# Kernel optimization log

Measured on AMD Instinct MI355X. Metric: run time of the kernel, lower is better.

## Reference

```python
import jax, jax.numpy as jnp
import numpy as np

DIM = 512
NUM_HEADS = 8
HEAD_DIM = DIM // NUM_HEADS
SCALE = HEAD_DIM ** -0.5


def setup_inputs() -> dict:
    key = jax.random.key(0)
    ks = jax.random.split(key, 11)
    B, T, D = 2, 4096, DIM
    s = 0.02
    return {
        "query": jax.random.normal(ks[0], (B, T, D), jnp.float32),
        "key_": jax.random.normal(ks[1], (B, T, D), jnp.float32),
        "value": jax.random.normal(ks[2], (B, T, D), jnp.float32),
        "Wq": jax.random.normal(ks[3], (D, D), jnp.float32) * s,
        "bq": jnp.zeros((D,), jnp.float32),
        "Wk": jax.random.normal(ks[4], (D, D), jnp.float32) * s,
        "bk": jnp.zeros((D,), jnp.float32),
        "Wv": jax.random.normal(ks[5], (D, D), jnp.float32) * s,
        "bv": jnp.zeros((D,), jnp.float32),
        "Wo": jax.random.normal(ks[6], (D, D), jnp.float32) * s,
        "bo": jnp.zeros((D,), jnp.float32),
    }


def reference(query, key_, value, Wq, bq, Wk, bk, Wv, bv, Wo, bo):
    B, T, D = query.shape
    H, Hd = NUM_HEADS, HEAD_DIM
    # Linear projections (torch Linear: x @ W.T + b)
    q = (query @ Wq.T + bq).reshape(B, T, H, Hd).transpose(0, 2, 1, 3)   # [B,H,T,Hd]
    k = (key_ @ Wk.T + bk).reshape(B, -1, H, Hd).transpose(0, 2, 1, 3)    # [B,H,S,Hd]
    v = (value @ Wv.T + bv).reshape(B, -1, H, Hd).transpose(0, 2, 1, 3)   # [B,H,S,Hd]
    # Full O(T*S) score matrix, as in the original (non-fused) module
    scores = jnp.einsum("bhtd,bhsd->bhts", q, k) * SCALE                  # [B,H,T,S]
    weights = jax.nn.softmax(scores, axis=-1)
    out = jnp.einsum("bhts,bhsd->bhtd", weights, v)                       # [B,H,T,Hd]
    out = out.transpose(0, 2, 1, 3).reshape(B, T, D)
    return out @ Wo.T + bo
```

## Files before the change

kernel.cpp:

```cpp
#include <hip/hip_runtime.h>
#include <cstdint>
#include <cstddef>

typedef __attribute__((ext_vector_type(8)))  __bf16 bf16x8;
typedef __attribute__((ext_vector_type(4)))  float  f32x4;
typedef __attribute__((ext_vector_type(16))) float  f32x16;
typedef __attribute__((ext_vector_type(8)))  unsigned short us8;

#define MFMA(a, b, c)   __builtin_amdgcn_mfma_f32_16x16x32_bf16((a), (b), (c), 0, 0, 0)
#define MFMA32(a, b, c) __builtin_amdgcn_mfma_f32_32x32x16_bf16((a), (b), (c), 0, 0, 0)

#define QSCALE 0.18033688011112042f

__device__ __forceinline__ unsigned short f2bf(float f) {
  unsigned u = __float_as_uint(f);
  u += 0x7fffu + ((u >> 16) & 1u);
  return (unsigned short)(u >> 16);
}

__device__ __forceinline__ float bf2f(unsigned short s) {
  unsigned u = ((unsigned)s) << 16;
  return __uint_as_float(u);
}

__device__ __forceinline__ unsigned cvtpk(float lo, float hi) {
  unsigned r;
  asm("v_cvt_pk_bf16_f32 %0, %1, %2" : "=v"(r) : "v"(lo), "v"(hi));
  return r;
}

__device__ __forceinline__ void pl32swap(unsigned& a, unsigned& b) {
  asm("v_permlane32_swap_b32 %0, %1" : "+v"(a), "+v"(b));
}

__device__ __forceinline__ void gload16(const void* g, void* l) {
  __builtin_amdgcn_global_load_lds(
      (__attribute__((address_space(1))) unsigned int*)(uintptr_t)g,
      (__attribute__((address_space(3))) unsigned int*)l,
      16, 0, 0);
}

__device__ __forceinline__ float tree16(const float* p) {
  float a = (p[0] + p[1]) + (p[2] + p[3]);
  float b = (p[4] + p[5]) + (p[6] + p[7]);
  float c = (p[8] + p[9]) + (p[10] + p[11]);
  float d = (p[12] + p[13]) + (p[14] + p[15]);
  return (a + b) + (c + d);
}

struct CastArgs {
  const float*    src[7];
  unsigned short* dst[7];
};
__global__ __launch_bounds__(256) void cast_kernel(CastArgs a) {
  const int i = blockIdx.x * 256 + threadIdx.x;
  int z, off;
  if (i < 3145728) { z = i >> 20;            off = i & 1048575; }
  else             { int j = i - 3145728; z = 3 + (j >> 16); off = j & 65535; }
  float4 f = ((const float4*)a.src[z])[off];
  ushort4 r;
  r.x = f2bf(f.x); r.y = f2bf(f.y); r.z = f2bf(f.z); r.w = f2bf(f.w);
  ((ushort4*)a.dst[z])[off] = r;
}

struct ProjArgs {
  const unsigned short* X[3];
  const unsigned short* W[3];
  const float*          bias[3];
  unsigned short*       out[3];
};

__global__ __launch_bounds__(256) void proj_qkv_kernel(ProjArgs args) {
  __shared__ alignas(16) unsigned short smem[3 * 8192];

  const int z = blockIdx.z;
  const unsigned short* __restrict__ X   = args.X[z];
  const unsigned short* __restrict__ W   = args.W[z];
  const float* __restrict__ bias         = args.bias[z];
  unsigned short* __restrict__ out       = args.out[z];
  const float scl = (z == 0) ? QSCALE : 1.0f;

  const int t = threadIdx.x;
  const int w = t >> 6, lane = t & 63;
  const int quad = lane >> 4, l15 = lane & 15;
  const int wr = w >> 1, wc = w & 1;
  const int m0 = blockIdx.x * 128, n0 = blockIdx.y * 128;

  const int srow = t >> 2;
  const int scol = (((t & 3) ^ (srow & 3)) << 3);

  f32x4 acc[4][4] = {};

#define STAGEP(idx, kk)                                                        \
  {                                                                            \
    unsigned short* nA = smem + (idx) * 8192;                                  \
    unsigned short* nB = nA + 4096;                                            \
    gload16(X + (size_t)(m0 + srow) * 512 + (kk) + scol,      &nA[w * 512]);   \
    gload16(X + (size_t)(m0 + srow + 64) * 512 + (kk) + scol, &nA[2048 + w * 512]); \
    gload16(W + (size_t)(n0 + srow) * 512 + (kk) + scol,      &nB[w * 512]);   \
    gload16(W + (size_t)(n0 + srow + 64) * 512 + (kk) + scol, &nB[2048 + w * 512]); \
  }

  STAGEP(0, 0);
  STAGEP(1, 32);

#pragma unroll
  for (int k0 = 0; k0 < 512; k0 += 32) {
    const int bi = (k0 >> 5) % 3;
    unsigned short* sA = smem + bi * 8192;
    unsigned short* sB = sA + 4096;
    if (k0 < 448) {
      STAGEP((bi + 2) % 3, k0 + 64);
      asm volatile("s_waitcnt vmcnt(8)" ::: "memory");
    } else if (k0 == 448) {
      asm volatile("s_waitcnt vmcnt(4)" ::: "memory");
    } else {
      asm volatile("s_waitcnt vmcnt(0)" ::: "memory");
    }
    __builtin_amdgcn_s_barrier();
    asm volatile("" ::: "memory");

    bf16x8 af[4], bfr[4];
#pragma unroll
    for (int mt = 0; mt < 4; ++mt) {
      int ra = wr * 64 + mt * 16 + l15;
      af[mt] = *(const bf16x8*)&sA[ra * 32 + ((quad ^ (ra & 3)) << 3)];
    }
#pragma unroll
    for (int nt = 0; nt < 4; ++nt) {
      int rb = wc * 64 + nt * 16 + l15;
      bfr[nt] = *(const bf16x8*)&sB[rb * 32 + ((quad ^ (rb & 3)) << 3)];
    }
#pragma unroll
    for (int mt = 0; mt < 4; ++mt)
#pragma unroll
      for (int nt = 0; nt < 4; ++nt)
        acc[mt][nt] = MFMA(af[mt], bfr[nt], acc[mt][nt]);

    asm volatile("" ::: "memory");
    __builtin_amdgcn_s_barrier();
  }
#undef STAGEP

  if (z != 2) {
#pragma unroll
    for (int nt = 0; nt < 4; ++nt) {
      int n = n0 + wc * 64 + nt * 16 + l15;
      float bv = bias[n];
      int h = n >> 6, hd = n & 63;
#pragma unroll
      for (int mt = 0; mt < 4; ++mt) {
#pragma unroll
        for (int r = 0; r < 4; ++r) {
          int m = m0 + wr * 64 + mt * 16 + quad * 4 + r;
          int b = m >> 12, tt = m & 4095;
          out[(((size_t)(b * 8 + h)) * 4096 + tt) * 64 + hd] =
              f2bf((acc[mt][nt][r] + bv) * scl);
        }
      }
    }
  } else {
    const int b   = m0 >> 12;
    const int tt0 = m0 & 4095;
#pragma unroll
    for (int h2 = 0; h2 < 2; ++h2) {
      __syncthreads();
      if (wc == h2) {
#pragma unroll
        for (int nt = 0; nt < 4; ++nt) {
          int nl = nt * 16 + l15;
          float bv = bias[n0 + h2 * 64 + nl];
#pragma unroll
          for (int mt = 0; mt < 4; ++mt)
#pragma unroll
            for (int r = 0; r < 4; ++r) {
              int ml = wr * 64 + mt * 16 + quad * 4 + r;
              smem[nl * 136 + ml] = f2bf((acc[mt][nt][r] + bv) * scl);
            }
        }
      }
      __syncthreads();
      const int row = t >> 2;
      const int c4  = (t & 3) * 8;
      const int n   = n0 + h2 * 64 + row;
      unsigned short* dst = out + ((size_t)(b * 512 + n)) * 4096 + tt0;
#pragma unroll
      for (int k = 0; k < 4; ++k)
        *(us8*)(dst + c4 + k * 32) = *(const us8*)&smem[row * 136 + c4 + k * 32];
    }
  }
}

__global__ __launch_bounds__(256) void proj_out_kernel(
    const unsigned short* __restrict__ P0, const unsigned short* __restrict__ P1,
    const float* __restrict__ pL, const unsigned short* __restrict__ W,
    const float* __restrict__ bias, float* __restrict__ out) {
  __shared__ alignas(16) unsigned short sA[2][2048];
  __shared__ alignas(16) unsigned short sB[3][4096];
  __shared__ float invL[512];

  const int t = threadIdx.x;
  const int w = t >> 6, lane = t & 63;
  const int quad = lane >> 4, l15 = lane & 15;
  const int m0 = blockIdx.x * 64, n0 = blockIdx.y * 128;
  const int b  = m0 >> 12, tt0 = m0 & 4095;

  {
    const int hh = t >> 5;
    const int r2 = (t & 31) * 2;
#pragma unroll
    for (int i = 0; i < 2; ++i) {
      const int row = r2 + i;
      const size_t ix = (size_t)(b * 8 + hh) * 4096 + tt0 + row;
      invL[hh * 64 + row] = 1.0f / (pL[ix] + pL[65536 + ix]);
    }
  }

  const int arow = t >> 2, ac = t & 3;
  const int srow = t >> 2;
  const int scol = (((t & 3) ^ (srow & 3)) << 3);

  __syncthreads();

  {
    us8 a0 = *(const us8*)&P0[(size_t)(m0 + arow) * 512 + ac * 8];
    us8 a1 = *(const us8*)&P1[(size_t)(m0 + arow) * 512 + ac * 8];
    const float inv = invL[arow];
    unsigned o[4];
#pragma unroll
    for (int i = 0; i < 4; ++i)
      o[i] = cvtpk((bf2f(a0[2 * i]) + bf2f(a1[2 * i])) * inv,
                   (bf2f(a0[2 * i + 1]) + bf2f(a1[2 * i + 1])) * inv);
    *(us8*)&sA[0][arow * 32 + ((ac ^ (arow & 3)) << 3)] = *(us8*)o;
    gload16(W + (size_t)(n0 + srow) * 512 + scol,      &sB[0][w * 512]);
    gload16(W + (size_t)(n0 + srow + 64) * 512 + scol, &sB[0][2048 + w * 512]);
    gload16(W + (size_t)(n0 + srow) * 512 + 32 + scol,      &sB[1][w * 512]);
    gload16(W + (size_t)(n0 + srow + 64) * 512 + 32 + scol, &sB[1][2048 + w * 512]);
  }
  __syncthreads();

  f32x4 acc[4][2] = {};

#pragma unroll
  for (int k0 = 0; k0 < 512; k0 += 32) {
    const int ba = (k0 >> 5) & 1;
    const int bb = (k0 >> 5) % 3;

    us8 a0n = {}, a1n = {};
    float invn = 0.f;
    if (k0 < 480) {
      const int kn = k0 + 32;
      a0n = *(const us8*)&P0[(size_t)(m0 + arow) * 512 + kn + ac * 8];
      a1n = *(const us8*)&P1[(size_t)(m0 + arow) * 512 + kn + ac * 8];
      invn = invL[(kn >> 6) * 64 + arow];
    }
    if (k0 < 448) {
      const int kn2 = k0 + 64;
      gload16(W + (size_t)(n0 + srow) * 512 + kn2 + scol,      &sB[(bb + 2) % 3][w * 512]);
      gload16(W + (size_t)(n0 + srow + 64) * 512 + kn2 + scol, &sB[(bb + 2) % 3][2048 + w * 512]);
    }

    bf16x8 af[4], bfr[2];
#pragma unroll
    for (int mt = 0; mt < 4; ++mt) {
      int ra = mt * 16 + l15;
      af[mt] = *(const bf16x8*)&sA[ba][ra * 32 + ((quad ^ (ra & 3)) << 3)];
    }
#pragma unroll
    for (int nt = 0; nt < 2; ++nt) {
      int rb = w * 32 + nt * 16 + l15;
      bfr[nt] = *(const bf16x8*)&sB[bb][rb * 32 + ((quad ^ (rb & 3)) << 3)];
    }
#pragma unroll
    for (int mt = 0; mt < 4; ++mt)
#pragma unroll
      for (int nt = 0; nt < 2; ++nt)
        acc[mt][nt] = MFMA(af[mt], bfr[nt], acc[mt][nt]);

    if (k0 < 480) {
      unsigned o[4];
#pragma unroll
      for (int i = 0; i < 4; ++i)
        o[i] = cvtpk((bf2f(a0n[2 * i]) + bf2f(a1n[2 * i])) * invn,
                     (bf2f(a0n[2 * i + 1]) + bf2f(a1n[2 * i + 1])) * invn);
      *(us8*)&sA[ba ^ 1][arow * 32 + ((ac ^ (arow & 3)) << 3)] = *(us8*)o;
    }

    asm volatile("s_waitcnt vmcnt(2) lgkmcnt(0)" ::: "memory");
    __builtin_amdgcn_s_barrier();
  }

#pragma unroll
  for (int nt = 0; nt < 2; ++nt) {
    int n = n0 + w * 32 + nt * 16 + l15;
    float bv = bias[n];
#pragma unroll
    for (int mt = 0; mt < 4; ++mt) {
#pragma unroll
      for (int r = 0; r < 4; ++r) {
        int m = m0 + mt * 16 + quad * 4 + r;
        out[(size_t)m * 512 + n] = acc[mt][nt][r] + bv;
      }
    }
  }
}

__global__ __launch_bounds__(128, 2) void attn_kernel(
    const unsigned short* __restrict__ Q, const unsigned short* __restrict__ K,
    const unsigned short* __restrict__ VT,
    unsigned short* __restrict__ pO0, unsigned short* __restrict__ pO1,
    float* __restrict__ pL) {
  __shared__ alignas(16) unsigned short kt[2][4096];
  __shared__ alignas(16) unsigned short vt[2][4096];

  const int t = threadIdx.x;
  const int w = t >> 6;
  const int lane = t & 63;
  const int l31 = lane & 31, h = lane >> 5;

  const int wg  = blockIdx.x + gridDim.x * blockIdx.y;
  const int swz = (wg & 7) * 128 + (wg >> 3);
  const int qt  = swz & 31;
  const int bh2 = swz >> 5;
  const int bh  = bh2 & 15, half = bh2 >> 4;

  const unsigned short* __restrict__ Qp  = Q  + (size_t)bh * 4096 * 64;
  const unsigned short* __restrict__ Kp  = K  + (size_t)bh * 4096 * 64;
  const unsigned short* __restrict__ VTp = VT + (size_t)bh * 64 * 4096;

  const int q0w = qt * 128 + w * 64;
  const int sbase = half * 2048;

  const int lr   = lane >> 3;
  const int gcol = (((lane & 7) ^ lr) << 3);

#define STAGE(bbuf, s0)                                                        \
  {                                                                            \
    _Pragma("unroll")                                                          \
    for (int i = 0; i < 4; ++i)                                                \
      gload16(Kp + (size_t)((s0) + w * 32 + i * 8 + lr) * 64 + gcol,           \
              &kt[bbuf][(w * 32 + i * 8) * 64]);                               \
    _Pragma("unroll")                                                          \
    for (int i = 0; i < 4; ++i)                                                \
      gload16(VTp + (size_t)(w * 32 + i * 8 + lr) * 4096 + (s0) + gcol,        \
              &vt[bbuf][(w * 32 + i * 8) * 64]);                               \
  }

  STAGE(0, sbase);

  bf16x8 aqA[4], aqB[4];
#pragma unroll
  for (int kd = 0; kd < 4; ++kd) {
    aqA[kd] = *(const bf16x8*)(Qp + (size_t)(q0w + l31) * 64 + kd * 16 + h * 8);
    aqB[kd] = *(const bf16x8*)(Qp + (size_t)(q0w + 32 + l31) * 64 + kd * 16 + h * 8);
  }

  f32x16 o0a = {}, o1a = {}, o0b = {}, o1b = {};
  float lia = 0.f, lib = 0.f;

  const int swzk = l31 & 7;

  for (int j = 0; j < 32; ++j) {
    const int cb = j & 1, nb = cb ^ 1;
    if (j < 31) {
      STAGE(nb, sbase + (j + 1) * 64);
      asm volatile("s_waitcnt vmcnt(8)" ::: "memory");
    } else {
      asm volatile("s_waitcnt vmcnt(0)" ::: "memory");
    }
    __builtin_amdgcn_s_barrier();
    asm volatile("" ::: "memory");

    const unsigned short* ktb = kt[cb];
    const unsigned short* vtb = vt[cb];

#pragma unroll
    for (int st = 0; st < 2; ++st) {
      bf16x8 kf[4];
#pragma unroll
      for (int kd = 0; kd < 4; ++kd)
        kf[kd] = *(const bf16x8*)&ktb[(st * 32 + l31) * 64 +
                                      (((2 * kd + h) ^ swzk) << 3)];
      f32x16 sa = {}, sb = {};
      __builtin_amdgcn_s_setprio(1);
#pragma unroll
      for (int kd = 0; kd < 4; ++kd) {
        sa = MFMA32(kf[kd], aqA[kd], sa);
        sb = MFMA32(kf[kd], aqB[kd], sb);
      }
      __builtin_amdgcn_s_setprio(0);

      float pA[16], pB[16];
#pragma unroll
      for (int r = 0; r < 16; ++r) {
        pA[r] = __builtin_amdgcn_exp2f(sa[r]);
        pB[r] = __builtin_amdgcn_exp2f(sb[r]);
      }
      lia += tree16(pA);
      lib += tree16(pB);

      unsigned XgA[4], YgA[4], XgB[4], YgB[4];
#pragma unroll
      for (int g = 0; g < 4; ++g) {
        XgA[g] = cvtpk(pA[4 * g + 0], pA[4 * g + 1]);
        YgA[g] = cvtpk(pA[4 * g + 2], pA[4 * g + 3]);
        XgB[g] = cvtpk(pB[4 * g + 0], pB[4 * g + 1]);
        YgB[g] = cvtpk(pB[4 * g + 2], pB[4 * g + 3]);
      }

      __builtin_amdgcn_s_setprio(1);
#pragma unroll
      for (int ks = 0; ks < 2; ++ks) {
        const int c = st * 4 + 2 * ks + h;
        bf16x8 v0 = *(const bf16x8*)&vtb[l31 * 64 + ((c ^ swzk) << 3)];
        bf16x8 v1 = *(const bf16x8*)&vtb[(l31 + 32) * 64 + ((c ^ swzk) << 3)];

        unsigned a0 = XgA[2 * ks], a2 = XgA[2 * ks + 1];
        unsigned a1 = YgA[2 * ks], a3 = YgA[2 * ks + 1];
        pl32swap(a0, a2);
        pl32swap(a1, a3);
        union { unsigned u[4]; bf16x8 v; } paA;
        paA.u[0] = a0; paA.u[1] = a1; paA.u[2] = a2; paA.u[3] = a3;
        o0a = MFMA32(paA.v, v0, o0a);
        o1a = MFMA32(paA.v, v1, o1a);

        unsigned b0 = XgB[2 * ks], b2 = XgB[2 * ks + 1];
        unsigned b1 = YgB[2 * ks], b3 = YgB[2 * ks + 1];
        pl32swap(b0, b2);
        pl32swap(b1, b3);
        union { unsigned u[4]; bf16x8 v; } paB;
        paB.u[0] = b0; paB.u[1] = b1; paB.u[2] = b2; paB.u[3] = b3;
        o0b = MFMA32(paB.v, v0, o0b);
        o1b = MFMA32(paB.v, v1, o1b);
      }
      __builtin_amdgcn_s_setprio(0);
    }

    asm volatile("" ::: "memory");
    __builtin_amdgcn_s_barrier();
  }
#undef STAGE

  lia += __shfl_xor(lia, 32, 64);
  lib += __shfl_xor(lib, 32, 64);
  float* __restrict__ PLh = pL + half * 65536 + bh * 4096;
  if (h == 0) {
    PLh[q0w + l31]      = lia;
    PLh[q0w + 32 + l31] = lib;
  }

  unsigned short* __restrict__ PO = half ? pO1 : pO0;
  const int bq = bh >> 3, hh = bh & 7;
#pragma unroll
  for (int r = 0; r < 16; ++r) {
    const int qloc = (r & 3) + 8 * (r >> 2) + 4 * h;
    const size_t baseA = ((size_t)bq * 4096 + q0w + qloc) * 512 + hh * 64;
    PO[baseA + l31]      = f2bf(o0a[r]);
    PO[baseA + 32 + l31] = f2bf(o1a[r]);
    const size_t baseB = ((size_t)bq * 4096 + q0w + 32 + qloc) * 512 + hh * 64;
    PO[baseB + l31]      = f2bf(o0b[r]);
    PO[baseB + 32 + l31] = f2bf(o1b[r]);
  }
}

extern "C" void kernel_launch(void* const* d_in, const int* in_sizes, int n_in,
                              void* d_out, int out_size, void* d_ws, size_t ws_size,
                              hipStream_t stream) {
  (void)in_sizes; (void)n_in; (void)out_size; (void)ws_size;
  const float* query = (const float*)d_in[0];
  const float* key_  = (const float*)d_in[1];
  const float* value = (const float*)d_in[2];
  const float* Wq = (const float*)d_in[3];
  const float* bq = (const float*)d_in[4];
  const float* Wk = (const float*)d_in[5];
  const float* bk = (const float*)d_in[6];
  const float* Wv = (const float*)d_in[7];
  const float* bv = (const float*)d_in[8];
  const float* Wo = (const float*)d_in[9];
  const float* bo = (const float*)d_in[10];
  float* out = (float*)d_out;

  char* ws = (char*)d_ws;
  const size_t MB = 1024 * 1024;
  unsigned short* Xq  = (unsigned short*)(ws + 0 * MB);
  unsigned short* Xk  = (unsigned short*)(ws + 8 * MB);
  unsigned short* Xv  = (unsigned short*)(ws + 16 * MB);
  unsigned short* Wqb = (unsigned short*)(ws + 24 * MB);
  unsigned short* Wkb = (unsigned short*)(ws + 24 * MB + 512 * 1024);
  unsigned short* Wvb = (unsigned short*)(ws + 25 * MB);
  unsigned short* qb  = (unsigned short*)(ws + 26 * MB);
  unsigned short* kb  = (unsigned short*)(ws + 34 * MB);
  unsigned short* vtb = (unsigned short*)(ws + 42 * MB);
  unsigned short* Wob = (unsigned short*)(ws + 58 * MB);
  unsigned short* pO0 = (unsigned short*)(ws + 0 * MB);
  unsigned short* pO1 = (unsigned short*)(ws + 9 * MB);
  float*          pL  = (float*)(ws + 18 * MB);

  CastArgs ca;
  ca.src[0] = query; ca.src[1] = key_; ca.src[2] = value;
  ca.src[3] = Wq;    ca.src[4] = Wk;   ca.src[5] = Wv;  ca.src[6] = Wo;
  ca.dst[0] = Xq;    ca.dst[1] = Xk;   ca.dst[2] = Xv;
  ca.dst[3] = Wqb;   ca.dst[4] = Wkb;  ca.dst[5] = Wvb; ca.dst[6] = Wob;
  cast_kernel<<<dim3(13312), 256, 0, stream>>>(ca);

  ProjArgs pa;
  pa.X[0] = Xq;  pa.X[1] = Xk;  pa.X[2] = Xv;
  pa.W[0] = Wqb; pa.W[1] = Wkb; pa.W[2] = Wvb;
  pa.bias[0] = bq; pa.bias[1] = bk; pa.bias[2] = bv;
  pa.out[0] = qb; pa.out[1] = kb; pa.out[2] = vtb;
  proj_qkv_kernel<<<dim3(64, 4, 3), 256, 0, stream>>>(pa);

  attn_kernel<<<dim3(32, 32), 128, 0, stream>>>(qb, kb, vtb, pO0, pO1, pL);

  proj_out_kernel<<<dim3(128, 4), 256, 0, stream>>>(pO0, pO1, pL, Wob, bo, out);
}
```

Baseline: 219.6 us.

## Fuse fp32-to-bf16 activation cast into QKV projection loads

The separate cast kernel no longer converts the large query/key/value activations. The projection kernel instead loads fp32 rows directly through registers, converts them to bf16 and writes them into a double-buffered LDS tile, while weights keep async global-to-LDS loads in a triple buffer. This removes a full write and re-read of the bf16 activation copies, at the cost of doubled fp32 global reads per tile and register-staged writes that may expose latency. The attention kernel's s_setprio raises around its MFMA blocks are also removed.

```diff
diff --git a/kernel.cpp b/kernel.cpp
--- a/kernel.cpp
+++ b/kernel.cpp
@@ -49,14 +49,12 @@
 }
 
 struct CastArgs {
-  const float*    src[7];
-  unsigned short* dst[7];
+  const float*    src[4];
+  unsigned short* dst[4];
 };
 __global__ __launch_bounds__(256) void cast_kernel(CastArgs a) {
   const int i = blockIdx.x * 256 + threadIdx.x;
-  int z, off;
-  if (i < 3145728) { z = i >> 20;            off = i & 1048575; }
-  else             { int j = i - 3145728; z = 3 + (j >> 16); off = j & 65535; }
+  const int z = i >> 16, off = i & 65535;
   float4 f = ((const float4*)a.src[z])[off];
   ushort4 r;
   r.x = f2bf(f.x); r.y = f2bf(f.y); r.z = f2bf(f.z); r.w = f2bf(f.w);
@@ -64,17 +62,19 @@
 }
 
 struct ProjArgs {
-  const unsigned short* X[3];
+  const float*          Xf[3];
   const unsigned short* W[3];
   const float*          bias[3];
   unsigned short*       out[3];
 };
 
 __global__ __launch_bounds__(256) void proj_qkv_kernel(ProjArgs args) {
-  __shared__ alignas(16) unsigned short smem[3 * 8192];
+  __shared__ alignas(16) unsigned short smem[20480];
+  unsigned short* sAb[2] = {smem, smem + 4096};
+  unsigned short* sBb[3] = {smem + 8192, smem + 12288, smem + 16384};
 
   const int z = blockIdx.z;
-  const unsigned short* __restrict__ X   = args.X[z];
+  const float* __restrict__ Xf           = args.Xf[z];
   const unsigned short* __restrict__ W   = args.W[z];
   const float* __restrict__ bias         = args.bias[z];
   unsigned short* __restrict__ out       = args.out[z];
@@ -86,50 +86,63 @@
   const int wr = w >> 1, wc = w & 1;
   const int m0 = blockIdx.x * 128, n0 = blockIdx.y * 128;
 
+  const int arow = t >> 2, ac = t & 3;
+  const int axc  = (ac ^ (arow & 3)) << 3;
   const int srow = t >> 2;
   const int scol = (((t & 3) ^ (srow & 3)) << 3);
 
   f32x4 acc[4][4] = {};
 
-#define STAGEP(idx, kk)                                                        \
+#define LOADX(va, vb, vc, vd, kk)                                              \
   {                                                                            \
-    unsigned short* nA = smem + (idx) * 8192;                                  \
-    unsigned short* nB = nA + 4096;                                            \
-    gload16(X + (size_t)(m0 + srow) * 512 + (kk) + scol,      &nA[w * 512]);   \
-    gload16(X + (size_t)(m0 + srow + 64) * 512 + (kk) + scol, &nA[2048 + w * 512]); \
-    gload16(W + (size_t)(n0 + srow) * 512 + (kk) + scol,      &nB[w * 512]);   \
-    gload16(W + (size_t)(n0 + srow + 64) * 512 + (kk) + scol, &nB[2048 + w * 512]); \
-  }
-
-  STAGEP(0, 0);
-  STAGEP(1, 32);
+    const float* p0 = Xf + (size_t)(m0 + arow) * 512 + (kk) + axc;             \
+    const float* p1 = Xf + (size_t)(m0 + arow + 64) * 512 + (kk) + axc;        \
+    va = *(const float4*)p0; vb = *(const float4*)(p0 + 4);                    \
+    vc = *(const float4*)p1; vd = *(const float4*)(p1 + 4);                    \
+  }
+#define WRITEX(buf, va, vb, vc, vd)                                            \
+  {                                                                            \
+    unsigned o0[4] = {cvtpk(va.x, va.y), cvtpk(va.z, va.w),                    \
+                      cvtpk(vb.x, vb.y), cvtpk(vb.z, vb.w)};                   \
+    unsigned o1[4] = {cvtpk(vc.x, vc.y), cvtpk(vc.z, vc.w),                    \
+                      cvtpk(vd.x, vd.y), cvtpk(vd.z, vd.w)};                   \
+    *(us8*)&sAb[buf][arow * 32 + (ac << 3)] = *(us8*)o0;                       \
+    *(us8*)&sAb[buf][(arow + 64) * 32 + (ac << 3)] = *(us8*)o1;                \
+  }
+#define LOADW(idx, kk)                                                         \
+  {                                                                            \
+    gload16(W + (size_t)(n0 + srow) * 512 + (kk) + scol,      &sBb[idx][w * 512]); \
+    gload16(W + (size_t)(n0 + srow + 64) * 512 + (kk) + scol, &sBb[idx][2048 + w * 512]); \
+  }
+
+  {
+    float4 va, vb, vc, vd;
+    LOADX(va, vb, vc, vd, 0);
+    WRITEX(0, va, vb, vc, vd);
+    LOADW(0, 0);
+    LOADW(1, 32);
+  }
+  __syncthreads();
 
 #pragma unroll
   for (int k0 = 0; k0 < 512; k0 += 32) {
-    const int bi = (k0 >> 5) % 3;
-    unsigned short* sA = smem + bi * 8192;
-    unsigned short* sB = sA + 4096;
-    if (k0 < 448) {
-      STAGEP((bi + 2) % 3, k0 + 64);
-      asm volatile("s_waitcnt vmcnt(8)" ::: "memory");
-    } else if (k0 == 448) {
-      asm volatile("s_waitcnt vmcnt(4)" ::: "memory");
-    } else {
-      asm volatile("s_waitcnt vmcnt(0)" ::: "memory");
-    }
-    __builtin_amdgcn_s_barrier();
-    asm volatile("" ::: "memory");
+    const int ba = (k0 >> 5) & 1;
+    const int bb = (k0 >> 5) % 3;
+
+    float4 va, vb, vc, vd;
+    if (k0 < 480) LOADX(va, vb, vc, vd, k0 + 32);
+    if (k0 < 448) LOADW((bb + 2) % 3, k0 + 64);
 
     bf16x8 af[4], bfr[4];
 #pragma unroll
     for (int mt = 0; mt < 4; ++mt) {
       int ra = wr * 64 + mt * 16 + l15;
-      af[mt] = *(const bf16x8*)&sA[ra * 32 + ((quad ^ (ra & 3)) << 3)];
+      af[mt] = *(const bf16x8*)&sAb[ba][ra * 32 + ((quad ^ (ra & 3)) << 3)];
     }
 #pragma unroll
     for (int nt = 0; nt < 4; ++nt) {
       int rb = wc * 64 + nt * 16 + l15;
-      bfr[nt] = *(const bf16x8*)&sB[rb * 32 + ((quad ^ (rb & 3)) << 3)];
+      bfr[nt] = *(const bf16x8*)&sBb[bb][rb * 32 + ((quad ^ (rb & 3)) << 3)];
     }
 #pragma unroll
     for (int mt = 0; mt < 4; ++mt)
@@ -137,10 +150,14 @@
       for (int nt = 0; nt < 4; ++nt)
         acc[mt][nt] = MFMA(af[mt], bfr[nt], acc[mt][nt]);
 
-    asm volatile("" ::: "memory");
+    if (k0 < 480) WRITEX(ba ^ 1, va, vb, vc, vd);
+
+    asm volatile("s_waitcnt vmcnt(2) lgkmcnt(0)" ::: "memory");
     __builtin_amdgcn_s_barrier();
   }
-#undef STAGEP
+#undef LOADX
+#undef WRITEX
+#undef LOADW
 
   if (z != 2) {
 #pragma unroll
@@ -382,13 +399,11 @@
         kf[kd] = *(const bf16x8*)&ktb[(st * 32 + l31) * 64 +
                                       (((2 * kd + h) ^ swzk) << 3)];
       f32x16 sa = {}, sb = {};
-      __builtin_amdgcn_s_setprio(1);
 #pragma unroll
       for (int kd = 0; kd < 4; ++kd) {
         sa = MFMA32(kf[kd], aqA[kd], sa);
         sb = MFMA32(kf[kd], aqB[kd], sb);
       }
-      __builtin_amdgcn_s_setprio(0);
 
       float pA[16], pB[16];
 #pragma unroll
@@ -408,7 +423,6 @@
         YgB[g] = cvtpk(pB[4 * g + 2], pB[4 * g + 3]);
       }
 
-      __builtin_amdgcn_s_setprio(1);
 #pragma unroll
       for (int ks = 0; ks < 2; ++ks) {
         const int c = st * 4 + 2 * ks + h;
@@ -433,7 +447,6 @@
         o0b = MFMA32(paB.v, v0, o0b);
         o1b = MFMA32(paB.v, v1, o1b);
       }
-      __builtin_amdgcn_s_setprio(0);
     }
 
     asm volatile("" ::: "memory");
@@ -482,29 +495,24 @@
 
   char* ws = (char*)d_ws;
   const size_t MB = 1024 * 1024;
-  unsigned short* Xq  = (unsigned short*)(ws + 0 * MB);
-  unsigned short* Xk  = (unsigned short*)(ws + 8 * MB);
-  unsigned short* Xv  = (unsigned short*)(ws + 16 * MB);
   unsigned short* Wqb = (unsigned short*)(ws + 24 * MB);
   unsigned short* Wkb = (unsigned short*)(ws + 24 * MB + 512 * 1024);
   unsigned short* Wvb = (unsigned short*)(ws + 25 * MB);
+  unsigned short* Wob = (unsigned short*)(ws + 58 * MB);
   unsigned short* qb  = (unsigned short*)(ws + 26 * MB);
   unsigned short* kb  = (unsigned short*)(ws + 34 * MB);
   unsigned short* vtb = (unsigned short*)(ws + 42 * MB);
-  unsigned short* Wob = (unsigned short*)(ws + 58 * MB);
   unsigned short* pO0 = (unsigned short*)(ws + 0 * MB);
   unsigned short* pO1 = (unsigned short*)(ws + 9 * MB);
   float*          pL  = (float*)(ws + 18 * MB);
 
   CastArgs ca;
-  ca.src[0] = query; ca.src[1] = key_; ca.src[2] = value;
-  ca.src[3] = Wq;    ca.src[4] = Wk;   ca.src[5] = Wv;  ca.src[6] = Wo;
-  ca.dst[0] = Xq;    ca.dst[1] = Xk;   ca.dst[2] = Xv;
-  ca.dst[3] = Wqb;   ca.dst[4] = Wkb;  ca.dst[5] = Wvb; ca.dst[6] = Wob;
-  cast_kernel<<<dim3(13312), 256, 0, stream>>>(ca);
+  ca.src[0] = Wq;  ca.src[1] = Wk;  ca.src[2] = Wv;  ca.src[3] = Wo;
+  ca.dst[0] = Wqb; ca.dst[1] = Wkb; ca.dst[2] = Wvb; ca.dst[3] = Wob;
+  cast_kernel<<<dim3(1024), 256, 0, stream>>>(ca);
 
   ProjArgs pa;
-  pa.X[0] = Xq;  pa.X[1] = Xk;  pa.X[2] = Xv;
+  pa.Xf[0] = query; pa.Xf[1] = key_; pa.Xf[2] = value;
   pa.W[0] = Wqb; pa.W[1] = Wkb; pa.W[2] = Wvb;
   pa.bias[0] = bq; pa.bias[1] = bk; pa.bias[2] = bv;
   pa.out[0] = qb; pa.out[1] = kb; pa.out[2] = vtb;
```

Result: slower. 228.1 us (+3.9%).
